# Kernel optimization log

Measured on AMD Instinct MI355X. Metric: run time of the kernel, lower is better.

## Reference

```python
import jax, jax.numpy as jnp
import numpy as np

B, T, I, H = 64, 512, 1024, 1024


def setup_inputs() -> dict:
    key = jax.random.key(0)
    k1, k2, k3, k4 = jax.random.split(key, 4)
    s_in = 1.0 / np.sqrt(I)
    s_h = 1.0 / np.sqrt(H)
    return {
        "x": jax.random.normal(k1, (B, T, I), dtype=jnp.float32),
        "Wih": jax.random.normal(k2, (4 * H, I), dtype=jnp.float32) * s_in,
        "Whh": jax.random.normal(k3, (4 * H, H), dtype=jnp.float32) * s_h,
        "b": jax.random.normal(k4, (4 * H,), dtype=jnp.float32) * s_h,
    }


def reference(x, Wih, Whh, b):
    """Sequential RNN layer (LSTM cell step) over (batch, seq_len, input).

    Mirrors RNNLayer.forward_tensor: zero-initialized state, per-timestep
    step(), stacked outputs plus final state. The Python time loop is
    expressed as a single lax.scan (one fused launch).
    """
    batch = x.shape[0]
    h0 = jnp.zeros((batch, H), dtype=x.dtype)
    c0 = jnp.zeros((batch, H), dtype=x.dtype)

    def step(carry, xt):  # xt: [B, I]
        h, c = carry
        gates = xt @ Wih.T + h @ Whh.T + b  # [B, 4H]
        i_g, f_g, g_g, o_g = jnp.split(gates, 4, axis=-1)
        c_new = jax.nn.sigmoid(f_g) * c + jax.nn.sigmoid(i_g) * jnp.tanh(g_g)
        h_new = jax.nn.sigmoid(o_g) * jnp.tanh(c_new)
        return (h_new, c_new), h_new

    xs = jnp.swapaxes(x, 0, 1)  # [T, B, I] for scan over time
    (h_T, c_T), outs = jax.lax.scan(step, (h0, c0), xs)
    outputs = jnp.swapaxes(outs, 0, 1)  # [B, T, H]
    return outputs, (h_T, c_T)
```

## Files before the change

kernel.cpp:

```cpp
#include <hip/hip_runtime.h>
#include <stdint.h>


typedef __bf16 bf16x8 __attribute__((ext_vector_type(8)));
typedef float f32x4 __attribute__((ext_vector_type(4)));

#define BATCH 64
#define TSEQ 512
#define HID 1024
#define MROWS (BATCH * TSEQ)
#define NGATE 4096

__device__ __forceinline__ unsigned short f2bf(float f) {
  union { float f; unsigned u; } v; v.f = f;
  unsigned r = (v.u + 0x7FFFu + ((v.u >> 16) & 1u)) >> 16;
  return (unsigned short)r;
}
__device__ __forceinline__ float bf2f(unsigned short u) {
  union { unsigned u; float f; } v; v.u = ((unsigned)u) << 16;
  return v.f;
}

__global__ void cvt_kernel(const float* __restrict__ src,
                           unsigned short* __restrict__ dst, int n4) {
  int i = blockIdx.x * blockDim.x + threadIdx.x;
  const int stride = gridDim.x * blockDim.x;
  for (; i < n4; i += stride) {
    float4 f = ((const float4*)src)[i];
    ushort4 u;
    u.x = f2bf(f.x); u.y = f2bf(f.y); u.z = f2bf(f.z); u.w = f2bf(f.w);
    ((ushort4*)dst)[i] = u;
  }
}

__device__ __forceinline__ void gl_lds16(const unsigned short* g, unsigned short* lds) {
  __builtin_amdgcn_global_load_lds(
      (const __attribute__((address_space(1))) unsigned int*)g,
      (__attribute__((address_space(3))) unsigned int*)lds, 16, 0, 0);
}

__global__ __launch_bounds__(256, 2) void gemm_xg(
    const unsigned short* __restrict__ A,
    const unsigned short* __restrict__ B,
    const float* __restrict__ bias,
    unsigned short* __restrict__ Xg)
{
  __shared__ __align__(16) unsigned short Asm[128 * 32];
  __shared__ __align__(16) unsigned short Bsm[128 * 32];
  const int tid = threadIdx.x;
  const int lane = tid & 63;
  const int wave = tid >> 6;
  const int row0 = blockIdx.y * 128;
  const int col0 = blockIdx.x * 128;
  const int wm = (wave >> 1) * 64;
  const int wn = (wave & 1) * 64;
  const int s_ml = lane >> 2;
  const int s_q = ((lane & 3) ^ (s_ml >> 1)) & 3;
  const int fm = lane & 15;
  const int fq = lane >> 4;
  const int swz = ((fq ^ (fm >> 1)) & 3) * 8;

  f32x4 acc[4][4] = {};

  for (int kt = 0; kt < 32; ++kt) {
    const int k0 = kt * 32;
    __syncthreads();
#pragma unroll
    for (int gI = 0; gI < 2; ++gI) {
      const int grp = wave * 2 + gI;
      const unsigned short* ga =
          A + (size_t)(row0 + grp * 16 + s_ml) * 1024 + k0 + s_q * 8;
      gl_lds16(ga, &Asm[grp * 512]);
      const unsigned short* gb =
          B + (size_t)(col0 + grp * 16 + s_ml) * 1024 + k0 + s_q * 8;
      gl_lds16(gb, &Bsm[grp * 512]);
    }
    __syncthreads();
    bf16x8 af[4], bfv[4];
#pragma unroll
    for (int mt = 0; mt < 4; ++mt) {
      const int m = wm + mt * 16 + fm;
      af[mt] = *(const bf16x8*)&Asm[(m >> 4) * 512 + fm * 32 + swz];
    }
#pragma unroll
    for (int nt = 0; nt < 4; ++nt) {
      const int n = wn + nt * 16 + fm;
      bfv[nt] = *(const bf16x8*)&Bsm[(n >> 4) * 512 + fm * 32 + swz];
    }
#pragma unroll
    for (int mt = 0; mt < 4; ++mt)
#pragma unroll
      for (int nt = 0; nt < 4; ++nt)
        acc[mt][nt] = __builtin_amdgcn_mfma_f32_16x16x32_bf16(
            af[mt], bfv[nt], acc[mt][nt], 0, 0, 0);
  }
#pragma unroll
  for (int nt = 0; nt < 4; ++nt) {
    const int nb = col0 + wn + nt * 16;
    const int pbase = ((nb & 1023) >> 4) * 64 + (nb >> 10) * 16;
    const float bv = bias[nb + fm];
#pragma unroll
    for (int mt = 0; mt < 4; ++mt) {
#pragma unroll
      for (int r = 0; r < 4; ++r) {
        const int row = row0 + wm + mt * 16 + fq * 4 + r;
        Xg[(size_t)row * 4096 + pbase + fm] = f2bf(acc[mt][nt][r] + bv);
      }
    }
  }
}

__device__ __forceinline__ bf16x8 load_h16B(const unsigned short* p) {
  union { unsigned long long q[2]; bf16x8 v; } u;
  const unsigned long long* q = (const unsigned long long*)p;
  u.q[0] = __hip_atomic_load(q, __ATOMIC_RELAXED, __HIP_MEMORY_SCOPE_AGENT);
  u.q[1] = __hip_atomic_load(q + 1, __ATOMIC_RELAXED, __HIP_MEMORY_SCOPE_AGENT);
  return u.v;
}

__global__ __launch_bounds__(256, 1) void lstm_seq(
    const unsigned short* __restrict__ Whh,
    const unsigned short* __restrict__ Xg,
    float* __restrict__ out,
    unsigned short* __restrict__ hbuf,
    unsigned int* __restrict__ counters)
{
  __shared__ float part[4][16][68];
  const int tid = threadIdx.x;
  const int lane = tid & 63;
  const int wave = tid >> 6;
  const int bn = blockIdx.x >> 2;
  const int mi = blockIdx.x & 3;
  const int fm = lane & 15;
  const int fq = lane >> 4;
  unsigned int* cnt = counters + mi * 256;

  bf16x8 bfrag[4][8];
#pragma unroll
  for (int g = 0; g < 4; ++g) {
    const unsigned short* wrow =
        Whh + (size_t)(g * 1024 + bn * 16 + fm) * 1024 + wave * 256 + fq * 8;
#pragma unroll
    for (int ki = 0; ki < 8; ++ki) bfrag[g][ki] = *(const bf16x8*)(wrow + ki * 32);
  }

  const int em = tid >> 4, ej = tid & 15;
  const int gb = mi * 16 + em;
  const int gj = bn * 16 + ej;
  float c_reg = 0.f;

  unsigned short* h0 = hbuf;
  unsigned short* h1 = hbuf + BATCH * HID;

  const unsigned short* xrow = Xg + (size_t)gb * TSEQ * 4096 + bn * 64;
  float xpre[4];
#pragma unroll
  for (int g = 0; g < 4; ++g) xpre[g] = bf2f(xrow[g * 16 + ej]);

  for (int t = 0; t < TSEQ; ++t) {
    const unsigned short* hp = (t & 1) ? h1 : h0;
    unsigned short* hn = (t & 1) ? h0 : h1;

    const unsigned short* ab =
        hp + (size_t)(mi * 16 + fm) * 1024 + wave * 256 + fq * 8;
    bf16x8 afr[8];
#pragma unroll
    for (int ki = 0; ki < 8; ++ki) afr[ki] = load_h16B(ab + ki * 32);

    f32x4 acc[4] = {};
#pragma unroll
    for (int ki = 0; ki < 8; ++ki)
#pragma unroll
      for (int g = 0; g < 4; ++g)
        acc[g] = __builtin_amdgcn_mfma_f32_16x16x32_bf16(afr[ki], bfrag[g][ki], acc[g], 0, 0, 0);

#pragma unroll
    for (int g = 0; g < 4; ++g)
#pragma unroll
      for (int r = 0; r < 4; ++r)
        part[wave][fq * 4 + r][g * 16 + fm] = acc[g][r];
    __syncthreads();

    float gate[4];
#pragma unroll
    for (int g = 0; g < 4; ++g) {
      float s = part[0][em][g * 16 + ej] + part[1][em][g * 16 + ej] +
                part[2][em][g * 16 + ej] + part[3][em][g * 16 + ej];
      gate[g] = s + xpre[g];
    }
    const float ig = 1.f / (1.f + __expf(-gate[0]));
    const float fg = 1.f / (1.f + __expf(-gate[1]));
    const float gg = 1.f - 2.f / (__expf(2.f * gate[2]) + 1.f);
    const float og = 1.f / (1.f + __expf(-gate[3]));
    c_reg = fg * c_reg + ig * gg;
    const float th = 1.f - 2.f / (__expf(2.f * c_reg) + 1.f);
    const float hv = og * th;

    __hip_atomic_store(&hn[(size_t)gb * HID + gj], f2bf(hv),
                       __ATOMIC_RELAXED, __HIP_MEMORY_SCOPE_AGENT);
    out[((size_t)gb * TSEQ + t) * HID + gj] = hv;

    if (t == TSEQ - 1) {
      out[(size_t)BATCH * TSEQ * HID + (size_t)gb * HID + gj] = hv;
      out[(size_t)BATCH * TSEQ * HID + (size_t)BATCH * HID + (size_t)gb * HID + gj] = c_reg;
      break;
    }
    {
      const unsigned short* xn = xrow + (size_t)(t + 1) * 4096;
#pragma unroll
      for (int g = 0; g < 4; ++g) xpre[g] = bf2f(xn[g * 16 + ej]);
    }

    __syncthreads();
    if (tid == 0) {
      __hip_atomic_fetch_add(&cnt[(bn & 7) * 32], 1u,
                             __ATOMIC_RELAXED, __HIP_MEMORY_SCOPE_AGENT);
      const unsigned target = 64u * (unsigned)(t + 1);
      for (;;) {
        unsigned s = 0;
#pragma unroll
        for (int i = 0; i < 8; ++i)
          s += __hip_atomic_load(&cnt[i * 32], __ATOMIC_RELAXED, __HIP_MEMORY_SCOPE_AGENT);
        if (s >= target) break;
        __builtin_amdgcn_s_sleep(1);
      }
    }
    __syncthreads();
  }
}

extern "C" void kernel_launch(void* const* d_in, const int* in_sizes, int n_in,
                              void* d_out, int out_size, void* d_ws, size_t ws_size,
                              hipStream_t stream) {
  (void)in_sizes; (void)n_in; (void)out_size;
  const float* x   = (const float*)d_in[0];
  const float* Wih = (const float*)d_in[1];
  const float* Whh = (const float*)d_in[2];
  const float* b   = (const float*)d_in[3];
  float* out = (float*)d_out;

  char* ws = (char*)d_ws;
  unsigned short* hbuf   = (unsigned short*)(ws + 1024);
  unsigned short* x_bf   = (unsigned short*)(ws + 263168);
  unsigned short* wih_bf = (unsigned short*)(ws + 263168 + 67108864);
  unsigned short* whh_bf = (unsigned short*)(ws + 263168 + 75497472);
  unsigned short* xg     = (unsigned short*)(ws + 263168 + 83886080);
  unsigned int* counters = (unsigned int*)x_bf;
  const size_t needed = 263168ULL + 83886080ULL + 268435456ULL;
  if (ws_size < needed) return;

  hipMemsetAsync(hbuf, 0, 2 * BATCH * HID * sizeof(unsigned short), stream);

  cvt_kernel<<<2048, 256, 0, stream>>>(x, x_bf, (MROWS * 1024) / 4);
  cvt_kernel<<<512, 256, 0, stream>>>(Wih, wih_bf, (NGATE * 1024) / 4);
  cvt_kernel<<<512, 256, 0, stream>>>(Whh, whh_bf, (NGATE * 1024) / 4);

  dim3 g(32, 256);
  gemm_xg<<<g, 256, 0, stream>>>(x_bf, wih_bf, b, xg);

  hipMemsetAsync(counters, 0, 4096, stream);

  lstm_seq<<<256, 256, 0, stream>>>(whh_bf, xg, out, hbuf, counters);
}
```

Baseline: 2.761 ms.

## Replace grid counter barrier with per-block flags and chunk-wise dataflow waits

Drops the per-step global barrier, where thread 0 sums eight shared counters. Each block now publishes its own step flag, and each wave polls only the flags of the producer blocks that own its K-slice of h. It then issues that slice's MFMAs as soon as the slice is ready, so the recurrent matmul overlaps with late producers. The output store moves after the flag publish, and the next-step Xg load is prefetched earlier, to take both off the critical path. In exchange the spin-polling traffic grows across many flag lines, and ordering still relies on relaxed atomics.

New measurement: 3.694 ms. +33.8%, slower.

```diff
diff --git a/kernel.cpp b/kernel.cpp
--- a/kernel.cpp
+++ b/kernel.cpp
@@ -123,7 +123,7 @@
     const unsigned short* __restrict__ Xg,
     float* __restrict__ out,
     unsigned short* __restrict__ hbuf,
-    unsigned int* __restrict__ counters)
+    unsigned int* __restrict__ flags)
 {
   __shared__ float part[4][16][68];
   const int tid = threadIdx.x;
@@ -133,7 +133,8 @@
   const int mi = blockIdx.x & 3;
   const int fm = lane & 15;
   const int fq = lane >> 4;
-  unsigned int* cnt = counters + mi * 256;
+  unsigned int* flg = flags + mi * 64 * 32;
+  unsigned int* myflag = flg + bn * 32;
 
   bf16x8 bfrag[4][8];
 #pragma unroll
@@ -160,19 +161,44 @@
   for (int t = 0; t < TSEQ; ++t) {
     const unsigned short* hp = (t & 1) ? h1 : h0;
     unsigned short* hn = (t & 1) ? h0 : h1;
-
     const unsigned short* ab =
         hp + (size_t)(mi * 16 + fm) * 1024 + wave * 256 + fq * 8;
-    bf16x8 afr[8];
-#pragma unroll
-    for (int ki = 0; ki < 8; ++ki) afr[ki] = load_h16B(ab + ki * 32);
+
+    float xcur[4];
+#pragma unroll
+    for (int g = 0; g < 4; ++g) xcur[g] = xpre[g];
+    if (t < TSEQ - 1) {
+      const unsigned short* xn = xrow + (size_t)(t + 1) * 4096;
+#pragma unroll
+      for (int g = 0; g < 4; ++g) xpre[g] = bf2f(xn[g * 16 + ej]);
+    }
 
     f32x4 acc[4] = {};
-#pragma unroll
-    for (int ki = 0; ki < 8; ++ki)
-#pragma unroll
-      for (int g = 0; g < 4; ++g)
-        acc[g] = __builtin_amdgcn_mfma_f32_16x16x32_bf16(afr[ki], bfrag[g][ki], acc[g], 0, 0, 0);
+    const unsigned need = (unsigned)t;
+    unsigned rem = 0xffu;
+    while (rem) {
+      unsigned prog = 0u;
+#pragma unroll
+      for (int ki = 0; ki < 8; ++ki) {
+        if (rem & (1u << ki)) {
+          const int p0 = wave * 16 + ki * 2;
+          const unsigned fa = __hip_atomic_load(&flg[p0 * 32], __ATOMIC_RELAXED,
+                                                __HIP_MEMORY_SCOPE_AGENT);
+          const unsigned fb = __hip_atomic_load(&flg[p0 * 32 + 32], __ATOMIC_RELAXED,
+                                                __HIP_MEMORY_SCOPE_AGENT);
+          if (fa >= need && fb >= need) {
+            const bf16x8 a = load_h16B(ab + ki * 32);
+#pragma unroll
+            for (int g = 0; g < 4; ++g)
+              acc[g] = __builtin_amdgcn_mfma_f32_16x16x32_bf16(a, bfrag[g][ki],
+                                                               acc[g], 0, 0, 0);
+            rem &= ~(1u << ki);
+            prog = 1u;
+          }
+        }
+      }
+      if (rem && !prog) __builtin_amdgcn_s_sleep(1);
+    }
 
 #pragma unroll
     for (int g = 0; g < 4; ++g)
@@ -186,7 +212,7 @@
     for (int g = 0; g < 4; ++g) {
       float s = part[0][em][g * 16 + ej] + part[1][em][g * 16 + ej] +
                 part[2][em][g * 16 + ej] + part[3][em][g * 16 + ej];
-      gate[g] = s + xpre[g];
+      gate[g] = s + xcur[g];
     }
     const float ig = 1.f / (1.f + __expf(-gate[0]));
     const float fg = 1.f / (1.f + __expf(-gate[1]));
@@ -198,34 +224,20 @@
 
     __hip_atomic_store(&hn[(size_t)gb * HID + gj], f2bf(hv),
                        __ATOMIC_RELAXED, __HIP_MEMORY_SCOPE_AGENT);
-    out[((size_t)gb * TSEQ + t) * HID + gj] = hv;
 
     if (t == TSEQ - 1) {
+      out[((size_t)gb * TSEQ + t) * HID + gj] = hv;
       out[(size_t)BATCH * TSEQ * HID + (size_t)gb * HID + gj] = hv;
       out[(size_t)BATCH * TSEQ * HID + (size_t)BATCH * HID + (size_t)gb * HID + gj] = c_reg;
       break;
     }
-    {
-      const unsigned short* xn = xrow + (size_t)(t + 1) * 4096;
-#pragma unroll
-      for (int g = 0; g < 4; ++g) xpre[g] = bf2f(xn[g * 16 + ej]);
-    }
-
-    __syncthreads();
-    if (tid == 0) {
-      __hip_atomic_fetch_add(&cnt[(bn & 7) * 32], 1u,
-                             __ATOMIC_RELAXED, __HIP_MEMORY_SCOPE_AGENT);
-      const unsigned target = 64u * (unsigned)(t + 1);
-      for (;;) {
-        unsigned s = 0;
-#pragma unroll
-        for (int i = 0; i < 8; ++i)
-          s += __hip_atomic_load(&cnt[i * 32], __ATOMIC_RELAXED, __HIP_MEMORY_SCOPE_AGENT);
-        if (s >= target) break;
-        __builtin_amdgcn_s_sleep(1);
-      }
-    }
-    __syncthreads();
+
+    __syncthreads();
+    if (tid == 0)
+      __hip_atomic_store(myflag, (unsigned)(t + 1),
+                         __ATOMIC_RELAXED, __HIP_MEMORY_SCOPE_AGENT);
+
+    out[((size_t)gb * TSEQ + t) * HID + gj] = hv;
   }
 }
 
@@ -245,7 +257,7 @@
   unsigned short* wih_bf = (unsigned short*)(ws + 263168 + 67108864);
   unsigned short* whh_bf = (unsigned short*)(ws + 263168 + 75497472);
   unsigned short* xg     = (unsigned short*)(ws + 263168 + 83886080);
-  unsigned int* counters = (unsigned int*)x_bf;
+  unsigned int* flags = (unsigned int*)x_bf;
   const size_t needed = 263168ULL + 83886080ULL + 268435456ULL;
   if (ws_size < needed) return;
 
@@ -258,7 +270,7 @@
   dim3 g(32, 256);
   gemm_xg<<<g, 256, 0, stream>>>(x_bf, wih_bf, b, xg);
 
-  hipMemsetAsync(counters, 0, 4096, stream);
-
-  lstm_seq<<<256, 256, 0, stream>>>(whh_bf, xg, out, hbuf, counters);
-}
+  hipMemsetAsync(flags, 0, 4 * 64 * 128, stream);
+
+  lstm_seq<<<256, 256, 0, stream>>>(whh_bf, xg, out, hbuf, flags);
+}
```
